# Optimization experiments

Hardware: AMD Instinct MI355X
Metric: run time of the kernel (lower is better)

Reference implementation:

```python
import jax, jax.numpy as jnp
import numpy as np

B, L, D, V, K = 8, 1024, 512, 64, 8
TEMP = 0.1
EPS = 1e-10
SPECIAL_IDS = (0, 1, 2, 3)  # pad, unk, bos, eos


def setup_inputs() -> dict:
    key = jax.random.key(0)
    ks = jax.random.split(key, 12)
    token_ids = jax.random.randint(ks[0], (B, L), 0, V, dtype=jnp.int32)
    # box_indices: prefix of valid targets in [L, 2L), padded with -1 (loop breaks at first -1)
    lengths = jax.random.randint(ks[1], (B, L, 1), 0, K + 1)
    tgt = jax.random.randint(ks[2], (B, L, K), L, 2 * L)
    box_indices = jnp.where(jnp.arange(K)[None, None, :] < lengths, tgt, -1).astype(jnp.int32)
    dtm_half = jax.random.uniform(ks[3], (B, L)) < 0.6
    data_tag_mask = jnp.concatenate([jnp.zeros((B, L), bool), dtm_half], axis=1)
    att_len = jax.random.randint(ks[4], (B, 1), L // 2, L + 1)
    att_half = jnp.arange(L)[None, :] < att_len
    attention_mask = jnp.concatenate([jnp.ones((B, L), bool), att_half], axis=1)
    tag_logits = jax.random.normal(ks[5], (B, L, V), dtype=jnp.float32)
    # scale projections so raw exp(logits/temperature) in the pointer loss stays finite
    box_proj = jax.random.normal(ks[6], (B, L, D), dtype=jnp.float32) * 0.05
    tag_proj = jax.random.normal(ks[7], (B, L, D), dtype=jnp.float32) * 0.05
    empty_proj = jax.random.normal(ks[8], (B, 1, D), dtype=jnp.float32) * 0.05
    row_sim_matrix = jax.random.normal(ks[9], (B, L, L), dtype=jnp.float32)
    col_sim_matrix = jax.random.normal(ks[10], (B, L, L), dtype=jnp.float32)
    u1, u2 = jax.random.uniform(ks[11], (2, B, L, L))
    # span coef: -1 = ignore, 0 = negative, (0,1] = weighted positive
    row_span_coef = jnp.where(u1 < 0.3, -1.0, jnp.where(u1 < 0.85, 0.0, u1))
    col_span_coef = jnp.where(u2 < 0.3, -1.0, jnp.where(u2 < 0.85, 0.0, u2))
    return {
        'token_ids': token_ids, 'box_indices': box_indices,
        'data_tag_mask': data_tag_mask, 'attention_mask': attention_mask,
        'tag_logits': tag_logits, 'box_proj': box_proj, 'tag_proj': tag_proj,
        'empty_proj': empty_proj, 'row_sim_matrix': row_sim_matrix,
        'col_sim_matrix': col_sim_matrix, 'row_span_coef': row_span_coef,
        'col_span_coef': col_span_coef,
    }


def _span_contrastive(sim, coef):
    # sim, coef: [B, N, N]
    n = sim.shape[-1]
    s = sim / TEMP
    s = s - jnp.max(s, axis=-1, keepdims=True)
    es = jnp.exp(s)
    idx = jnp.arange(n)
    den = es.sum(-1) - es[:, idx, idx]              # [B, N] denominator excludes self
    logden = jnp.log(den + EPS)                      # [B, N]
    pos = coef > 0
    w = jnp.where(pos, coef, 0.0)
    # -(coef * log(exp_sim / den)).sum / coef.sum  over positives
    num = (w * (logden[..., None] - s)).sum(-1)      # [B, N]
    loss_bj = num / (w.sum(-1) + EPS)
    has_pos = pos.any(-1)
    cnt = has_pos.sum()
    total = (jnp.where(has_pos, loss_bj, 0.0)).sum()
    return jnp.where(cnt > 0, total / jnp.maximum(cnt, 1), 0.0)


def reference(token_ids, box_indices, data_tag_mask, attention_mask,
              tag_logits, box_proj, tag_proj, empty_proj,
              row_sim_matrix, col_sim_matrix, row_span_coef, col_span_coef):
    Lp = box_proj.shape[1]  # layout_prompt_length == otsl_sequence_length
    # ---- cls loss: cross entropy with label_smoothing=0.1 over non-special tokens ----
    logp = jax.nn.log_softmax(tag_logits, axis=-1).reshape(-1, tag_logits.shape[-1])
    tt = token_ids.reshape(-1)
    nll = -jnp.take_along_axis(logp, tt[:, None].astype(jnp.int32), axis=1)[:, 0]
    smooth = -logp.mean(-1)
    per_tok = 0.9 * nll + 0.1 * smooth
    special = jnp.array(SPECIAL_IDS, dtype=tt.dtype)
    valid_tok = ~(tt[:, None] == special[None, :]).any(-1)
    cls_loss = (per_tok * valid_tok).sum() / jnp.maximum(valid_tok.sum(), 1)

    # ---- pointer loss ----
    dtm = data_tag_mask[:, Lp:]                                   # [B, T]
    logits = jnp.einsum('bld,btd->blt', box_proj, tag_proj) / TEMP  # [B, L, T]
    den = jnp.where(dtm[:, None, :], jnp.exp(logits), 0.0).sum(-1)  # [B, L]
    rel = box_indices - Lp                                        # [B, L, K]
    # loop breaks at first -1 -> valid targets are a contiguous prefix
    seq_valid = jnp.cumprod((box_indices != -1).astype(jnp.int32), axis=-1).astype(bool)
    rel_c = jnp.clip(rel, 0, logits.shape[-1] - 1)
    l_tgt = jnp.take_along_axis(logits, rel_c, axis=2)            # [B, L, K]
    dtm_g = jnp.take_along_axis(jnp.broadcast_to(dtm[:, None, :], logits.shape), rel_c, axis=2)
    m = seq_valid & dtm_g
    cnt = m.sum()
    terms = jnp.where(m, jnp.log(den + EPS)[..., None] - l_tgt, 0.0)
    ptr_loss = jnp.where(cnt > 0, terms.sum() / jnp.maximum(cnt, 1), 0.0)

    # ---- empty pointer loss (BCE with logits, no temperature) ----
    el = jnp.einsum('bd,btd->bt', empty_proj[:, 0, :], tag_proj)  # [B, T]
    att = attention_mask[:, Lp:]
    tgt_e = (att & ~dtm).astype(el.dtype)
    bce = jax.nn.softplus(el) - el * tgt_e
    per_b = (jnp.where(att, bce, 0.0)).sum(-1) / jnp.maximum(att.sum(-1), 1)
    empty_ptr_loss = per_b.mean()

    # ---- span-aware contrastive losses ----
    row_contr = _span_contrastive(row_sim_matrix, row_span_coef)
    col_contr = _span_contrastive(col_sim_matrix, col_span_coef)

    total = (1.0 * cls_loss + 1.0 * ptr_loss + 1.0 * empty_ptr_loss
             + 0.5 * row_contr + 0.5 * col_contr)
    return jnp.stack([total, cls_loss, ptr_loss, empty_ptr_loss, row_contr, col_contr])
```

## Files before the change

### kernel.cpp

```cpp
#include <hip/hip_runtime.h>
#include <hip/hip_bf16.h>
#include <math.h>

#define BB 8
#define LL 1024
#define DD 512
#define VV 64
#define KK 8

constexpr float INV_TEMP = 10.0f;
constexpr float EPSF     = 1e-10f;

#define WS_DENP   0
#define WS_CLS    (8192*8)
#define WS_EMP    (WS_CLS + 4096)
#define WS_CONTR  (WS_EMP + 4096)
#define WS_PTRROW (WS_CONTR + 8192)

typedef __attribute__((ext_vector_type(8))) short  short8;
typedef __attribute__((ext_vector_type(4))) float  f32x4;

__device__ __forceinline__ int mask_mode(const void* att_raw) {
    const unsigned* w = (const unsigned*)att_raw;
    unsigned w0 = w[0];
    if (w0 == 0x01010101u) return 0;
    if (w0 == 0x3f800000u) return 2;
    if (w0 == 1u) return (w[1] == 0u) ? 3 : 1;
    return 0;
}
__device__ __forceinline__ bool get_mask(const void* p, int idx, int mode) {
    if (mode == 0) return ((const unsigned char*)p)[idx] != 0;
    if (mode == 1) return ((const int*)p)[idx] != 0;
    if (mode == 3) return ((const unsigned*)p)[2*idx] != 0u;
    return ((const float*)p)[idx] != 0.0f;
}

__device__ __forceinline__ float wave_red_sum(float v) {
    #pragma unroll
    for (int off = 32; off; off >>= 1) v += __shfl_xor(v, off);
    return v;
}
__device__ __forceinline__ float wave_red_max(float v) {
    #pragma unroll
    for (int off = 32; off; off >>= 1) v = fmaxf(v, __shfl_xor(v, off));
    return v;
}

__device__ __forceinline__ short bfb(float f) {
    __hip_bfloat16 h = __float2bfloat16(f);
    union { __hip_bfloat16 h; short u; } c; c.h = h; return c.u;
}

#define BM 128
#define BKD 32
#define ST 40

__global__ __launch_bounds__(256) void k_den(const float* __restrict__ box,
                                             const float* __restrict__ tag,
                                             const void* __restrict__ dtm_raw,
                                             const void* __restrict__ att_raw,
                                             float* __restrict__ ws) {
    __shared__ short As[BM * ST];
    __shared__ short Bs[BM * ST];

    int bid   = blockIdx.x;
    int b     = bid & 7;
    int tile  = bid >> 3;
    int l0    = (tile >> 3) * BM;
    int ttile = tile & 7;
    int t0    = ttile * BM;

    int tid  = threadIdx.x;
    int lane = tid & 63;
    int wave = tid >> 6;
    int wr   = wave >> 1, wc = wave & 1;

    int srow  = tid >> 1;
    int shalf = tid & 1;
    const float* gA = box + ((size_t)b * LL + l0 + srow) * DD + shalf * 16;
    const float* gB = tag + ((size_t)b * LL + t0 + srow) * DD + shalf * 16;
    short* wA = &As[srow * ST + shalf * 16];
    short* wB = &Bs[srow * ST + shalf * 16];

    f32x4 acc[4][4];
    #pragma unroll
    for (int m = 0; m < 4; m++)
        #pragma unroll
        for (int n = 0; n < 4; n++) acc[m][n] = (f32x4){0.f, 0.f, 0.f, 0.f};

    int k0 = (lane >> 4) * 8;
    const short* rA = &As[(wr * 64 + (lane & 15)) * ST + k0];
    const short* rB = &Bs[(wc * 64 + (lane & 15)) * ST + k0];

    for (int d0 = 0; d0 < DD; d0 += BKD) {
        __syncthreads();
        float4 fa0 = *(const float4*)(gA + d0);
        float4 fa1 = *(const float4*)(gA + d0 + 4);
        float4 fa2 = *(const float4*)(gA + d0 + 8);
        float4 fa3 = *(const float4*)(gA + d0 + 12);
        float4 fb0 = *(const float4*)(gB + d0);
        float4 fb1 = *(const float4*)(gB + d0 + 4);
        float4 fb2 = *(const float4*)(gB + d0 + 8);
        float4 fb3 = *(const float4*)(gB + d0 + 12);
        short8 va0 = {bfb(fa0.x), bfb(fa0.y), bfb(fa0.z), bfb(fa0.w),
                      bfb(fa1.x), bfb(fa1.y), bfb(fa1.z), bfb(fa1.w)};
        short8 va1 = {bfb(fa2.x), bfb(fa2.y), bfb(fa2.z), bfb(fa2.w),
                      bfb(fa3.x), bfb(fa3.y), bfb(fa3.z), bfb(fa3.w)};
        short8 vb0 = {bfb(fb0.x), bfb(fb0.y), bfb(fb0.z), bfb(fb0.w),
                      bfb(fb1.x), bfb(fb1.y), bfb(fb1.z), bfb(fb1.w)};
        short8 vb1 = {bfb(fb2.x), bfb(fb2.y), bfb(fb2.z), bfb(fb2.w),
                      bfb(fb3.x), bfb(fb3.y), bfb(fb3.z), bfb(fb3.w)};
        *(short8*)wA       = va0;
        *(short8*)(wA + 8) = va1;
        *(short8*)wB       = vb0;
        *(short8*)(wB + 8) = vb1;
        __syncthreads();

        short8 af[4], bf[4];
        #pragma unroll
        for (int m = 0; m < 4; m++) af[m] = *(const short8*)(rA + m * 16 * ST);
        #pragma unroll
        for (int n = 0; n < 4; n++) bf[n] = *(const short8*)(rB + n * 16 * ST);
        #pragma unroll
        for (int m = 0; m < 4; m++)
            #pragma unroll
            for (int n = 0; n < 4; n++)
                acc[m][n] = __builtin_amdgcn_mfma_f32_16x16x32_bf16(af[m], bf[n], acc[m][n], 0, 0, 0);
    }

    int mode = mask_mode(att_raw);
    bool mk[4];
    #pragma unroll
    for (int n = 0; n < 4; n++) {
        int t = t0 + wc * 64 + n * 16 + (lane & 15);
        mk[n] = get_mask(dtm_raw, b * (2 * LL) + LL + t, mode);
    }
    #pragma unroll
    for (int m = 0; m < 4; m++) {
        #pragma unroll
        for (int reg = 0; reg < 4; reg++) {
            float s = 0.0f;
            #pragma unroll
            for (int n = 0; n < 4; n++)
                s += mk[n] ? __expf(acc[m][n][reg] * INV_TEMP) : 0.0f;
            #pragma unroll
            for (int off = 1; off < 16; off <<= 1) s += __shfl_xor(s, off);
            if ((lane & 15) == 0) {
                int l = l0 + wr * 64 + m * 16 + (lane >> 4) * 4 + reg;
                ws[WS_DENP + (b * LL + l) * 8 + ttile] = s;
            }
        }
    }
}

__global__ __launch_bounds__(256, 8) void k_light2(
        const float* __restrict__ box,     const float* __restrict__ tag,
        const float* __restrict__ logits,  const int* __restrict__ tok,
        const int* __restrict__ bidx,      const float* __restrict__ emptyp,
        const float* __restrict__ row_sim, const float* __restrict__ col_sim,
        const float* __restrict__ row_coef,const float* __restrict__ col_coef,
        const void* __restrict__ dtm_raw,  const void* __restrict__ att_raw,
        float* __restrict__ ws) {
    __shared__ float part[4][2];
    int bid  = blockIdx.x;
    int tid  = threadIdx.x;
    int lane = tid & 63;
    int wv   = tid >> 6;

    if (bid < 2048) {
        int b  = bid & 7;
        int li = bid >> 3;
        int i  = li * 4 + wv;
        int row = b * LL + i;
        int mode = mask_mode(att_raw);

        const float4* tp = (const float4*)(tag + (size_t)row * DD + lane * 8);
        const float4* ep = (const float4*)(emptyp + (size_t)b * DD + lane * 8);
        float4 t0v = tp[0], t1v = tp[1];
        float4 e0  = ep[0], e1  = ep[1];
        float de = e0.x * t0v.x + e0.y * t0v.y + e0.z * t0v.z + e0.w * t0v.w
                 + e1.x * t1v.x + e1.y * t1v.y + e1.z * t1v.z + e1.w * t1v.w;

        const float4* bp = (const float4*)(box + (size_t)row * DD + lane * 8);
        float4 x0 = bp[0], x1 = bp[1];
        float4 ya0 = {0.f,0.f,0.f,0.f}, ya1 = {0.f,0.f,0.f,0.f};
        float cnt = 0.0f;
        bool running = true;
        for (int k = 0; k < KK; k++) {
            int idx = bidx[row * KK + k];
            running = running && (idx != -1);
            int rel  = idx - LL;
            int relc = min(max(rel, 0), LL - 1);
            bool dg = get_mask(dtm_raw, b * (2 * LL) + LL + relc, mode);
            if (running && dg) {
                const float4* gp = (const float4*)(tag + ((size_t)b * LL + relc) * DD + lane * 8);
                float4 y0 = gp[0], y1 = gp[1];
                ya0.x += y0.x; ya0.y += y0.y; ya0.z += y0.z; ya0.w += y0.w;
                ya1.x += y1.x; ya1.y += y1.y; ya1.z += y1.z; ya1.w += y1.w;
                cnt += 1.0f;
            }
        }
        float dsum = x0.x * ya0.x + x0.y * ya0.y + x0.z * ya0.z + x0.w * ya0.w
                   + x1.x * ya1.x + x1.y * ya1.y + x1.z * ya1.z + x1.w * ya1.w;
        #pragma unroll
        for (int off = 32; off; off >>= 1) {
            dsum += __shfl_xor(dsum, off);
            de   += __shfl_xor(de,   off);
        }
        if (lane == 0) {
            ws[WS_PTRROW + row * 2 + 0] = dsum;
            ws[WS_PTRROW + row * 2 + 1] = cnt;
        }
        bool att = get_mask(att_raw, b * (2 * LL) + LL + i, mode);
        float bce = 0.0f, acnt = 0.0f;
        if (att) {
            bool dtm = get_mask(dtm_raw, b * (2 * LL) + LL + i, mode);
            float tgt = dtm ? 0.0f : 1.0f;
            float sp  = fmaxf(de, 0.0f) + log1pf(expf(-fabsf(de)));
            bce = sp - de * tgt;
            acnt = 1.0f;
        }
        if (lane == 0) { part[wv][0] = bce; part[wv][1] = acnt; }
        __syncthreads();
        if (tid == 0) {
            int slot = b * 256 + li;
            ws[WS_EMP + slot * 2 + 0] = part[0][0] + part[1][0] + part[2][0] + part[3][0];
            ws[WS_EMP + slot * 2 + 1] = part[0][1] + part[1][1] + part[2][1] + part[3][1];
        }
        return;
    }

    if (bid < 4096) {
        int cb = bid - 2048;
        int b  = cb & 7;
        int li = cb >> 3;
        int row = b * LL + li * 4 + wv;
        float x  = logits[(size_t)row * VV + lane];
        float mx = wave_red_max(x);
        float se = wave_red_sum(__expf(x - mx));
        float sx = wave_red_sum(x);
        float logZ = mx + logf(se);
        int t = tok[row];
        float xt = __shfl(x, t);
        float per = 0.9f * (logZ - xt) + 0.1f * (logZ - sx * (1.0f / VV));
        bool valid = (t > 3);
        if (lane == 0) {
            part[wv][0] = valid ? per : 0.0f;
            part[wv][1] = valid ? 1.0f : 0.0f;
        }
        __syncthreads();
        if (tid == 0) {
            ws[WS_CLS + cb * 2 + 0] = part[0][0] + part[1][0] + part[2][0] + part[3][0];
            ws[WS_CLS + cb * 2 + 1] = part[0][1] + part[1][1] + part[2][1] + part[3][1];
        }
        return;
    }

    {
        int cb   = bid - 4096;
        int gw   = cb * 4 + wv;
        int mat  = gw >> 13;
        int row  = gw & 8191;
        int j    = row & 1023;
        const float* sim  = (mat ? col_sim  : row_sim)  + (size_t)row * LL;
        const float* coef = (mat ? col_coef : row_coef) + (size_t)row * LL;

        float4 v[4], c[4];
        #pragma unroll
        for (int e = 0; e < 4; e++) v[e] = ((const float4*)sim)[e * 64 + lane];
        #pragma unroll
        for (int e = 0; e < 4; e++) c[e] = ((const float4*)coef)[e * 64 + lane];

        float se = 0.0f, diag = 0.0f, sw = 0.0f, sws = 0.0f;
        #pragma unroll
        for (int e = 0; e < 4; e++) {
            float xs[4] = {v[e].x, v[e].y, v[e].z, v[e].w};
            float cs[4] = {c[e].x, c[e].y, c[e].z, c[e].w};
            #pragma unroll
            for (int q = 0; q < 4; q++) {
                float s  = xs[q] * INV_TEMP;
                float es = __expf(s);
                se += es;
                if (e * 256 + lane * 4 + q == j) diag = es;
                float w = cs[q] > 0.0f ? cs[q] : 0.0f;
                sw  += w;
                sws += w * s;
            }
        }
        #pragma unroll
        for (int off = 32; off; off >>= 1) {
            se   += __shfl_xor(se,   off);
            diag += __shfl_xor(diag, off);
            sw   += __shfl_xor(sw,   off);
            sws  += __shfl_xor(sws,  off);
        }
        float logden = logf(se - diag + EPSF);
        bool hp = sw > 0.0f;
        float loss = (logden * sw - sws) / (sw + EPSF);
        if (lane == 0) {
            part[wv][0] = hp ? loss : 0.0f;
            part[wv][1] = hp ? 1.0f : 0.0f;
        }
        __syncthreads();
        if (tid == 0) {
            ws[WS_CONTR + cb * 2 + 0] = part[0][0] + part[1][0] + part[2][0] + part[3][0];
            ws[WS_CONTR + cb * 2 + 1] = part[0][1] + part[1][1] + part[2][1] + part[3][1];
        }
    }
}

__global__ __launch_bounds__(1024) void k_final(const float* __restrict__ ws, float* __restrict__ out) {
    __shared__ float red[16][12];
    int tid  = threadIdx.x;
    int lane = tid & 63, wv = tid >> 6;

    float q[12];
    #pragma unroll
    for (int i = 0; i < 12; i++) q[i] = 0.0f;

    #pragma unroll
    for (int i = 0; i < 8; i++) {
        int row = tid * 8 + i;
        const float* dp = ws + WS_DENP + (size_t)row * 8;
        float4 d0 = *(const float4*)dp;
        float4 d1 = *(const float4*)(dp + 4);
        float den = d0.x + d0.y + d0.z + d0.w + d1.x + d1.y + d1.z + d1.w;
        float sumd = ws[WS_PTRROW + row * 2 + 0];
        float cnt  = ws[WS_PTRROW + row * 2 + 1];
        q[2] += cnt * logf(den + EPSF) - INV_TEMP * sumd;
        q[3] += cnt;
    }
    #pragma unroll
    for (int it = 0; it < 2; it++) {
        int i = tid + it * 1024;
        q[0] += ws[WS_CLS + 2 * i];  q[1] += ws[WS_CLS + 2 * i + 1];
    }
    q[4] = ws[WS_CONTR + 2 * tid]              + ws[WS_CONTR + 2 * (tid + 1024)];
    q[5] = ws[WS_CONTR + 2 * tid + 1]          + ws[WS_CONTR + 2 * (tid + 1024) + 1];
    q[6] = ws[WS_CONTR + 2 * (tid + 2048)]     + ws[WS_CONTR + 2 * (tid + 3072)];
    q[7] = ws[WS_CONTR + 2 * (tid + 2048) + 1] + ws[WS_CONTR + 2 * (tid + 3072) + 1];
    q[8]  = ws[WS_EMP + 2 * tid];
    q[9]  = ws[WS_EMP + 2 * tid + 1];
    q[10] = ws[WS_EMP + 2 * (tid + 1024)];
    q[11] = ws[WS_EMP + 2 * (tid + 1024) + 1];

    #pragma unroll
    for (int i = 0; i < 12; i++) {
        #pragma unroll
        for (int off = 32; off; off >>= 1) q[i] += __shfl_xor(q[i], off);
    }
    if (lane == 0) {
        #pragma unroll
        for (int i = 0; i < 12; i++) red[wv][i] = q[i];
    }
    __syncthreads();
    if (tid == 0) {
        float s[8];
        #pragma unroll
        for (int i = 0; i < 8; i++) s[i] = 0.0f;
        float es[8], ec[8];
        #pragma unroll
        for (int i = 0; i < 8; i++) { es[i] = 0.0f; ec[i] = 0.0f; }
        #pragma unroll
        for (int w = 0; w < 16; w++) {
            #pragma unroll
            for (int i = 0; i < 8; i++) s[i] += red[w][i];
            es[(w >> 2)]     += red[w][8];
            ec[(w >> 2)]     += red[w][9];
            es[(w >> 2) + 4] += red[w][10];
            ec[(w >> 2) + 4] += red[w][11];
        }
        float cls = s[0] / fmaxf(s[1], 1.0f);
        float ptr = (s[3] > 0.0f) ? s[2] / fmaxf(s[3], 1.0f) : 0.0f;
        float emp = 0.0f;
        #pragma unroll
        for (int b = 0; b < 8; b++) emp += es[b] / fmaxf(ec[b], 1.0f);
        emp *= (1.0f / BB);
        float rc = (s[5] > 0.0f) ? s[4] / fmaxf(s[5], 1.0f) : 0.0f;
        float cc = (s[7] > 0.0f) ? s[6] / fmaxf(s[7], 1.0f) : 0.0f;
        float tot = cls + ptr + emp + 0.5f * (rc + cc);
        out[0] = tot; out[1] = cls; out[2] = ptr;
        out[3] = emp; out[4] = rc;  out[5] = cc;
    }
}

extern "C" void kernel_launch(void* const* d_in, const int* in_sizes, int n_in,
                              void* d_out, int out_size, void* d_ws, size_t ws_size,
                              hipStream_t stream) {
    (void)in_sizes; (void)n_in; (void)out_size; (void)ws_size;
    const int*   token_ids = (const int*)  d_in[0];
    const int*   box_idx   = (const int*)  d_in[1];
    const void*  dtm       =               d_in[2];
    const void*  att       =               d_in[3];
    const float* tag_log   = (const float*)d_in[4];
    const float* box_proj  = (const float*)d_in[5];
    const float* tag_proj  = (const float*)d_in[6];
    const float* empty_p   = (const float*)d_in[7];
    const float* row_sim   = (const float*)d_in[8];
    const float* col_sim   = (const float*)d_in[9];
    const float* row_coef  = (const float*)d_in[10];
    const float* col_coef  = (const float*)d_in[11];
    float* ws  = (float*)d_ws;
    float* out = (float*)d_out;

    k_den   <<<BB * 64, 256, 0, stream>>>(box_proj, tag_proj, dtm, att, ws);
    k_light2<<<8192, 256, 0, stream>>>(box_proj, tag_proj, tag_log, token_ids,
                                       box_idx, empty_p, row_sim, col_sim,
                                       row_coef, col_coef, dtm, att, ws);
    k_final <<<1, 1024, 0, stream>>>(ws, out);
}
```

Baseline: 75.77 us.

## Fuse GEMM denominator kernel into light kernel with interleaved block roles

Merges the separate MFMA denominator kernel into the main per-row kernel, so one launch interleaves contrastive, GEMM, pointer/empty and classification blocks in a fixed 20-block pattern. The GEMM tile shrinks from 128x128 to 64x64 (2048 blocks writing 16 partials per row instead of 8). The aim is to overlap compute-bound matmul work with the memory-bound contrastive streaming and to remove a launch boundary. Sim/coef loads become nontemporal. In exchange, smaller tiles re-read box/tag data more often, and the shared-memory footprint now applies to every block, which may reduce occupancy for the light roles.

```diff
diff --git a/kernel.cpp b/kernel.cpp
--- a/kernel.cpp
+++ b/kernel.cpp
@@ -12,7 +12,7 @@
 constexpr float EPSF     = 1e-10f;
 
 #define WS_DENP   0
-#define WS_CLS    (8192*8)
+#define WS_CLS    (8192*16)
 #define WS_EMP    (WS_CLS + 4096)
 #define WS_CONTR  (WS_EMP + 4096)
 #define WS_PTRROW (WS_CONTR + 8192)
@@ -51,109 +51,9 @@
     union { __hip_bfloat16 h; short u; } c; c.h = h; return c.u;
 }
 
-#define BM 128
-#define BKD 32
 #define ST 40
 
-__global__ __launch_bounds__(256) void k_den(const float* __restrict__ box,
-                                             const float* __restrict__ tag,
-                                             const void* __restrict__ dtm_raw,
-                                             const void* __restrict__ att_raw,
-                                             float* __restrict__ ws) {
-    __shared__ short As[BM * ST];
-    __shared__ short Bs[BM * ST];
-
-    int bid   = blockIdx.x;
-    int b     = bid & 7;
-    int tile  = bid >> 3;
-    int l0    = (tile >> 3) * BM;
-    int ttile = tile & 7;
-    int t0    = ttile * BM;
-
-    int tid  = threadIdx.x;
-    int lane = tid & 63;
-    int wave = tid >> 6;
-    int wr   = wave >> 1, wc = wave & 1;
-
-    int srow  = tid >> 1;
-    int shalf = tid & 1;
-    const float* gA = box + ((size_t)b * LL + l0 + srow) * DD + shalf * 16;
-    const float* gB = tag + ((size_t)b * LL + t0 + srow) * DD + shalf * 16;
-    short* wA = &As[srow * ST + shalf * 16];
-    short* wB = &Bs[srow * ST + shalf * 16];
-
-    f32x4 acc[4][4];
-    #pragma unroll
-    for (int m = 0; m < 4; m++)
-        #pragma unroll
-        for (int n = 0; n < 4; n++) acc[m][n] = (f32x4){0.f, 0.f, 0.f, 0.f};
-
-    int k0 = (lane >> 4) * 8;
-    const short* rA = &As[(wr * 64 + (lane & 15)) * ST + k0];
-    const short* rB = &Bs[(wc * 64 + (lane & 15)) * ST + k0];
-
-    for (int d0 = 0; d0 < DD; d0 += BKD) {
-        __syncthreads();
-        float4 fa0 = *(const float4*)(gA + d0);
-        float4 fa1 = *(const float4*)(gA + d0 + 4);
-        float4 fa2 = *(const float4*)(gA + d0 + 8);
-        float4 fa3 = *(const float4*)(gA + d0 + 12);
-        float4 fb0 = *(const float4*)(gB + d0);
-        float4 fb1 = *(const float4*)(gB + d0 + 4);
-        float4 fb2 = *(const float4*)(gB + d0 + 8);
-        float4 fb3 = *(const float4*)(gB + d0 + 12);
-        short8 va0 = {bfb(fa0.x), bfb(fa0.y), bfb(fa0.z), bfb(fa0.w),
-                      bfb(fa1.x), bfb(fa1.y), bfb(fa1.z), bfb(fa1.w)};
-        short8 va1 = {bfb(fa2.x), bfb(fa2.y), bfb(fa2.z), bfb(fa2.w),
-                      bfb(fa3.x), bfb(fa3.y), bfb(fa3.z), bfb(fa3.w)};
-        short8 vb0 = {bfb(fb0.x), bfb(fb0.y), bfb(fb0.z), bfb(fb0.w),
-                      bfb(fb1.x), bfb(fb1.y), bfb(fb1.z), bfb(fb1.w)};
-        short8 vb1 = {bfb(fb2.x), bfb(fb2.y), bfb(fb2.z), bfb(fb2.w),
-                      bfb(fb3.x), bfb(fb3.y), bfb(fb3.z), bfb(fb3.w)};
-        *(short8*)wA       = va0;
-        *(short8*)(wA + 8) = va1;
-        *(short8*)wB       = vb0;
-        *(short8*)(wB + 8) = vb1;
-        __syncthreads();
-
-        short8 af[4], bf[4];
-        #pragma unroll
-        for (int m = 0; m < 4; m++) af[m] = *(const short8*)(rA + m * 16 * ST);
-        #pragma unroll
-        for (int n = 0; n < 4; n++) bf[n] = *(const short8*)(rB + n * 16 * ST);
-        #pragma unroll
-        for (int m = 0; m < 4; m++)
-            #pragma unroll
-            for (int n = 0; n < 4; n++)
-                acc[m][n] = __builtin_amdgcn_mfma_f32_16x16x32_bf16(af[m], bf[n], acc[m][n], 0, 0, 0);
-    }
-
-    int mode = mask_mode(att_raw);
-    bool mk[4];
-    #pragma unroll
-    for (int n = 0; n < 4; n++) {
-        int t = t0 + wc * 64 + n * 16 + (lane & 15);
-        mk[n] = get_mask(dtm_raw, b * (2 * LL) + LL + t, mode);
-    }
-    #pragma unroll
-    for (int m = 0; m < 4; m++) {
-        #pragma unroll
-        for (int reg = 0; reg < 4; reg++) {
-            float s = 0.0f;
-            #pragma unroll
-            for (int n = 0; n < 4; n++)
-                s += mk[n] ? __expf(acc[m][n][reg] * INV_TEMP) : 0.0f;
-            #pragma unroll
-            for (int off = 1; off < 16; off <<= 1) s += __shfl_xor(s, off);
-            if ((lane & 15) == 0) {
-                int l = l0 + wr * 64 + m * 16 + (lane >> 4) * 4 + reg;
-                ws[WS_DENP + (b * LL + l) * 8 + ttile] = s;
-            }
-        }
-    }
-}
-
-__global__ __launch_bounds__(256, 8) void k_light2(
+__global__ __launch_bounds__(256, 8) void k_mega(
         const float* __restrict__ box,     const float* __restrict__ tag,
         const float* __restrict__ logits,  const int* __restrict__ tok,
         const int* __restrict__ bidx,      const float* __restrict__ emptyp,
@@ -161,15 +61,150 @@
         const float* __restrict__ row_coef,const float* __restrict__ col_coef,
         const void* __restrict__ dtm_raw,  const void* __restrict__ att_raw,
         float* __restrict__ ws) {
-    __shared__ float part[4][2];
-    int bid  = blockIdx.x;
+    __shared__ short As[64 * ST];
+    __shared__ short Bs[64 * ST];
+
+    int bid = blockIdx.x;
+    int g   = bid / 20;
+    int r   = bid - g * 20;
     int tid  = threadIdx.x;
     int lane = tid & 63;
     int wv   = tid >> 6;
 
-    if (bid < 2048) {
+    if (r < 8) {
+        int cidx = g * 8 + r;
+        int gw   = cidx * 4 + wv;
+        int mat  = gw >> 13;
+        int row  = gw & 8191;
+        int j    = row & 1023;
+        const f32x4* sim  = (const f32x4*)((mat ? col_sim  : row_sim)  + (size_t)row * LL);
+        const f32x4* coef = (const f32x4*)((mat ? col_coef : row_coef) + (size_t)row * LL);
+
+        f32x4 v[4], c[4];
+        #pragma unroll
+        for (int e = 0; e < 4; e++) v[e] = __builtin_nontemporal_load(sim + e * 64 + lane);
+        #pragma unroll
+        for (int e = 0; e < 4; e++) c[e] = __builtin_nontemporal_load(coef + e * 64 + lane);
+
+        float se = 0.0f, diag = 0.0f, sw = 0.0f, sws = 0.0f;
+        #pragma unroll
+        for (int e = 0; e < 4; e++) {
+            #pragma unroll
+            for (int q = 0; q < 4; q++) {
+                float s  = v[e][q] * INV_TEMP;
+                float es = __expf(s);
+                se += es;
+                if (e * 256 + lane * 4 + q == j) diag = es;
+                float cw = c[e][q];
+                float w = cw > 0.0f ? cw : 0.0f;
+                sw  += w;
+                sws += w * s;
+            }
+        }
+        #pragma unroll
+        for (int off = 32; off; off >>= 1) {
+            se   += __shfl_xor(se,   off);
+            diag += __shfl_xor(diag, off);
+            sw   += __shfl_xor(sw,   off);
+            sws  += __shfl_xor(sws,  off);
+        }
+        float logden = logf(se - diag + EPSF);
+        bool hp = sw > 0.0f;
+        float loss = (logden * sw - sws) / (sw + EPSF);
+        float (*part)[2] = (float(*)[2])As;
+        if (lane == 0) {
+            part[wv][0] = hp ? loss : 0.0f;
+            part[wv][1] = hp ? 1.0f : 0.0f;
+        }
+        __syncthreads();
+        if (tid == 0) {
+            ws[WS_CONTR + cidx * 2 + 0] = part[0][0] + part[1][0] + part[2][0] + part[3][0];
+            ws[WS_CONTR + cidx * 2 + 1] = part[0][1] + part[1][1] + part[2][1] + part[3][1];
+        }
+        return;
+    }
+
+    if (r < 12) {
+        int b   = bid & 7;
+        int idx = g >> 1;
+        int lt  = idx >> 4, tt = idx & 15;
+        int l0  = lt * 64,  t0 = tt * 64;
+        int wr  = wv >> 1,  wc = wv & 1;
+
+        int srow = tid >> 2;
+        int sq   = tid & 3;
+        const float* gA = box + ((size_t)b * LL + l0 + srow) * DD + sq * 8;
+        const float* gB = tag + ((size_t)b * LL + t0 + srow) * DD + sq * 8;
+        short* wA = &As[srow * ST + sq * 8];
+        short* wB = &Bs[srow * ST + sq * 8];
+
+        f32x4 acc[2][2];
+        #pragma unroll
+        for (int m = 0; m < 2; m++)
+            #pragma unroll
+            for (int n = 0; n < 2; n++) acc[m][n] = (f32x4){0.f, 0.f, 0.f, 0.f};
+
+        const short* rA = &As[(wr * 32 + (lane & 15)) * ST + (lane >> 4) * 8];
+        const short* rB = &Bs[(wc * 32 + (lane & 15)) * ST + (lane >> 4) * 8];
+
+        for (int d0 = 0; d0 < DD; d0 += 32) {
+            __syncthreads();
+            float4 fa0 = *(const float4*)(gA + d0);
+            float4 fa1 = *(const float4*)(gA + d0 + 4);
+            float4 fb0 = *(const float4*)(gB + d0);
+            float4 fb1 = *(const float4*)(gB + d0 + 4);
+            short8 va = {bfb(fa0.x), bfb(fa0.y), bfb(fa0.z), bfb(fa0.w),
+                         bfb(fa1.x), bfb(fa1.y), bfb(fa1.z), bfb(fa1.w)};
+            short8 vb = {bfb(fb0.x), bfb(fb0.y), bfb(fb0.z), bfb(fb0.w),
+                         bfb(fb1.x), bfb(fb1.y), bfb(fb1.z), bfb(fb1.w)};
+            *(short8*)wA = va;
+            *(short8*)wB = vb;
+            __syncthreads();
+
+            short8 af0 = *(const short8*)rA;
+            short8 af1 = *(const short8*)(rA + 16 * ST);
+            short8 bf0 = *(const short8*)rB;
+            short8 bf1 = *(const short8*)(rB + 16 * ST);
+            acc[0][0] = __builtin_amdgcn_mfma_f32_16x16x32_bf16(af0, bf0, acc[0][0], 0, 0, 0);
+            acc[0][1] = __builtin_amdgcn_mfma_f32_16x16x32_bf16(af0, bf1, acc[0][1], 0, 0, 0);
+            acc[1][0] = __builtin_amdgcn_mfma_f32_16x16x32_bf16(af1, bf0, acc[1][0], 0, 0, 0);
+            acc[1][1] = __builtin_amdgcn_mfma_f32_16x16x32_bf16(af1, bf1, acc[1][1], 0, 0, 0);
+        }
+
+        int mode = mask_mode(att_raw);
+        bool mk[2];
+        #pragma unroll
+        for (int n = 0; n < 2; n++) {
+            int t = t0 + wc * 32 + n * 16 + (lane & 15);
+            mk[n] = get_mask(dtm_raw, b * (2 * LL) + LL + t, mode);
+        }
+        __syncthreads();
+        float* part = (float*)As;
+        #pragma unroll
+        for (int m = 0; m < 2; m++) {
+            #pragma unroll
+            for (int reg = 0; reg < 4; reg++) {
+                float s = (mk[0] ? __expf(acc[m][0][reg] * INV_TEMP) : 0.0f)
+                        + (mk[1] ? __expf(acc[m][1][reg] * INV_TEMP) : 0.0f);
+                #pragma unroll
+                for (int off = 1; off < 16; off <<= 1) s += __shfl_xor(s, off);
+                if ((lane & 15) == 0) {
+                    int rl = wr * 32 + m * 16 + (lane >> 4) * 4 + reg;
+                    part[rl * 2 + wc] = s;
+                }
+            }
+        }
+        __syncthreads();
+        if (tid < 64) {
+            float s = part[tid * 2] + part[tid * 2 + 1];
+            ws[WS_DENP + ((size_t)b * LL + l0 + tid) * 16 + tt] = s;
+        }
+        return;
+    }
+
+    if (r < 16) {
         int b  = bid & 7;
-        int li = bid >> 3;
+        int li = g >> 1;
         int i  = li * 4 + wv;
         int row = b * LL + i;
         int mode = mask_mode(att_raw);
@@ -220,6 +255,7 @@
             bce = sp - de * tgt;
             acnt = 1.0f;
         }
+        float (*part)[2] = (float(*)[2])As;
         if (lane == 0) { part[wv][0] = bce; part[wv][1] = acnt; }
         __syncthreads();
         if (tid == 0) {
@@ -230,11 +266,9 @@
         return;
     }
 
-    if (bid < 4096) {
-        int cb = bid - 2048;
-        int b  = cb & 7;
-        int li = cb >> 3;
-        int row = b * LL + li * 4 + wv;
+    {
+        int cb  = g * 4 + (r - 16);
+        int row = cb * 4 + wv;
         float x  = logits[(size_t)row * VV + lane];
         float mx = wave_red_max(x);
         float se = wave_red_sum(__expf(x - mx));
@@ -244,6 +278,7 @@
         float xt = __shfl(x, t);
         float per = 0.9f * (logZ - xt) + 0.1f * (logZ - sx * (1.0f / VV));
         bool valid = (t > 3);
+        float (*part)[2] = (float(*)[2])As;
         if (lane == 0) {
             part[wv][0] = valid ? per : 0.0f;
             part[wv][1] = valid ? 1.0f : 0.0f;
@@ -252,59 +287,6 @@
         if (tid == 0) {
             ws[WS_CLS + cb * 2 + 0] = part[0][0] + part[1][0] + part[2][0] + part[3][0];
             ws[WS_CLS + cb * 2 + 1] = part[0][1] + part[1][1] + part[2][1] + part[3][1];
-        }
-        return;
-    }
-
-    {
-        int cb   = bid - 4096;
-        int gw   = cb * 4 + wv;
-        int mat  = gw >> 13;
-        int row  = gw & 8191;
-        int j    = row & 1023;
-        const float* sim  = (mat ? col_sim  : row_sim)  + (size_t)row * LL;
-        const float* coef = (mat ? col_coef : row_coef) + (size_t)row * LL;
-
-        float4 v[4], c[4];
-        #pragma unroll
-        for (int e = 0; e < 4; e++) v[e] = ((const float4*)sim)[e * 64 + lane];
-        #pragma unroll
-        for (int e = 0; e < 4; e++) c[e] = ((const float4*)coef)[e * 64 + lane];
-
-        float se = 0.0f, diag = 0.0f, sw = 0.0f, sws = 0.0f;
-        #pragma unroll
-        for (int e = 0; e < 4; e++) {
-            float xs[4] = {v[e].x, v[e].y, v[e].z, v[e].w};
-            float cs[4] = {c[e].x, c[e].y, c[e].z, c[e].w};
-            #pragma unroll
-            for (int q = 0; q < 4; q++) {
-                float s  = xs[q] * INV_TEMP;
-                float es = __expf(s);
-                se += es;
-                if (e * 256 + lane * 4 + q == j) diag = es;
-                float w = cs[q] > 0.0f ? cs[q] : 0.0f;
-                sw  += w;
-                sws += w * s;
-            }
-        }
-        #pragma unroll
-        for (int off = 32; off; off >>= 1) {
-            se   += __shfl_xor(se,   off);
-            diag += __shfl_xor(diag, off);
-            sw   += __shfl_xor(sw,   off);
-            sws  += __shfl_xor(sws,  off);
-        }
-        float logden = logf(se - diag + EPSF);
-        bool hp = sw > 0.0f;
-        float loss = (logden * sw - sws) / (sw + EPSF);
-        if (lane == 0) {
-            part[wv][0] = hp ? loss : 0.0f;
-            part[wv][1] = hp ? 1.0f : 0.0f;
-        }
-        __syncthreads();
-        if (tid == 0) {
-            ws[WS_CONTR + cb * 2 + 0] = part[0][0] + part[1][0] + part[2][0] + part[3][0];
-            ws[WS_CONTR + cb * 2 + 1] = part[0][1] + part[1][1] + part[2][1] + part[3][1];
         }
     }
 }
@@ -321,10 +303,13 @@
     #pragma unroll
     for (int i = 0; i < 8; i++) {
         int row = tid * 8 + i;
-        const float* dp = ws + WS_DENP + (size_t)row * 8;
-        float4 d0 = *(const float4*)dp;
-        float4 d1 = *(const float4*)(dp + 4);
-        float den = d0.x + d0.y + d0.z + d0.w + d1.x + d1.y + d1.z + d1.w;
+        const float* dp = ws + WS_DENP + (size_t)row * 16;
+        float den = 0.0f;
+        #pragma unroll
+        for (int p = 0; p < 4; p++) {
+            float4 d = *(const float4*)(dp + p * 4);
+            den += d.x + d.y + d.z + d.w;
+        }
         float sumd = ws[WS_PTRROW + row * 2 + 0];
         float cnt  = ws[WS_PTRROW + row * 2 + 1];
         q[2] += cnt * logf(den + EPSF) - INV_TEMP * sumd;
@@ -403,9 +388,8 @@
     float* ws  = (float*)d_ws;
     float* out = (float*)d_out;
 
-    k_den   <<<BB * 64, 256, 0, stream>>>(box_proj, tag_proj, dtm, att, ws);
-    k_light2<<<8192, 256, 0, stream>>>(box_proj, tag_proj, tag_log, token_ids,
-                                       box_idx, empty_p, row_sim, col_sim,
-                                       row_coef, col_coef, dtm, att, ws);
-    k_final <<<1, 1024, 0, stream>>>(ws, out);
-}
+    k_mega <<<512 * 20, 256, 0, stream>>>(box_proj, tag_proj, tag_log, token_ids,
+                                          box_idx, empty_p, row_sim, col_sim,
+                                          row_coef, col_coef, dtm, att, ws);
+    k_final<<<1, 1024, 0, stream>>>(ws, out);
+}
```

Result: slower. 81.73 us (+7.9%).
